# Optimization experiments

Hardware: AMD Instinct MI355X
Metric: run time of the kernel (lower is better)

## Reference

```python
import jax, jax.numpy as jnp
import numpy as np

HEAD = 16
EMB = 1024
D_K = EMB // HEAD


def setup_inputs() -> dict:
    key = jax.random.key(0)
    ks = jax.random.split(key, 11)
    B, S, E = 2, 2048, EMB
    scale = 1.0 / np.sqrt(E)
    inp = {
        "query": jax.random.normal(ks[0], (B, S, E), jnp.float32),
        "key": jax.random.normal(ks[1], (B, S, E), jnp.float32),
        "value": jax.random.normal(ks[2], (B, S, E), jnp.float32),
        "Wq": jax.random.normal(ks[3], (E, E), jnp.float32) * scale,
        "bq": jnp.zeros((E,), jnp.float32),
        "Wk": jax.random.normal(ks[4], (E, E), jnp.float32) * scale,
        "bk": jnp.zeros((E,), jnp.float32),
        "Wv": jax.random.normal(ks[5], (E, E), jnp.float32) * scale,
        "bv": jnp.zeros((E,), jnp.float32),
        "Wo": jax.random.normal(ks[6], (E, E), jnp.float32) * scale,
        "bo": jnp.zeros((E,), jnp.float32),
    }
    return inp


def reference(query, key, value, Wq, bq, Wk, bk, Wv, bv, Wo, bo):
    B, S, E = query.shape
    # 3 input projections, split into heads: [B, H, S, d_k]
    def proj(x, W, b):
        return (x @ W.T + b).reshape(B, S, HEAD, D_K).transpose(0, 2, 1, 3)

    q = proj(query, Wq, bq)
    k = proj(key, Wk, bk)
    v = proj(value, Wv, bv)

    # scaled dot-product attention (full matrix, as in original)
    scores = jnp.einsum("bhqd,bhkd->bhqk", q, k) / jnp.sqrt(jnp.float32(D_K))
    attn = jax.nn.softmax(scores, axis=-1)  # dropout in eval mode = identity
    x = jnp.einsum("bhqk,bhkd->bhqd", attn, v)

    # merge heads and output projection
    x = x.transpose(0, 2, 1, 3).reshape(B, S, E)
    return x @ Wo.T + bo
```

## Files before the change

kernel.cpp:

```cpp
#include <hip/hip_runtime.h>
#include <hip/hip_bf16.h>
#include <math.h>


constexpr int Sn = 2048;
constexpr int En = 1024;
constexpr int Hn = 16;
constexpr int Dk = 64;
constexpr int Kn = 1024;
constexpr size_t WSZ = 1048576;
constexpr size_t TSZ = 4194304;
constexpr int PST = 72;

typedef __bf16 bf16x8 __attribute__((ext_vector_type(8)));
typedef float  f32x4  __attribute__((ext_vector_type(4)));

union U16 { uint4 u; bf16x8 v; __hip_bfloat16 h[8]; };
union U8  { uint2 u; __hip_bfloat162 h2[2]; __hip_bfloat16 h[4]; };

__device__ inline U16 cvt8f(const float* __restrict__ p) {
    float4 a = *(const float4*)p;
    float4 b = *(const float4*)(p + 4);
    U16 r;
    r.h[0] = __float2bfloat16(a.x); r.h[1] = __float2bfloat16(a.y);
    r.h[2] = __float2bfloat16(a.z); r.h[3] = __float2bfloat16(a.w);
    r.h[4] = __float2bfloat16(b.x); r.h[5] = __float2bfloat16(b.y);
    r.h[6] = __float2bfloat16(b.z); r.h[7] = __float2bfloat16(b.w);
    return r;
}

__device__ inline void gload16(const __hip_bfloat16* g, __hip_bfloat16* l) {
    __builtin_amdgcn_global_load_lds(
        (const __attribute__((address_space(1))) void*)g,
        (__attribute__((address_space(3))) void*)l, 16, 0, 0);
}

template<int ROWS, int NW>
__device__ inline void stage_tile(const __hip_bfloat16* __restrict__ src, int ld,
                                  __hip_bfloat16* lds, int w, int lane) {
    int l8 = lane >> 3;
    int g = (lane & 7) ^ (l8 & 7);
    #pragma unroll
    for (int j = 0; j < ROWS / (8 * NW); ++j) {
        int c = j * NW + w;
        gload16(src + (size_t)(c * 8 + l8) * ld + g * 8, lds + c * 512);
    }
}

__global__ __launch_bounds__(256)
void cvt_w(const float* __restrict__ w0, const float* __restrict__ w1,
           const float* __restrict__ w2, const float* __restrict__ w3,
           __hip_bfloat16* __restrict__ dst)
{
    int y = blockIdx.y;
    const float* src = (y == 0) ? w0 : (y == 1) ? w1 : (y == 2) ? w2 : w3;
    size_t i = ((size_t)blockIdx.x * 256 + threadIdx.x) * 8;
    U16 r = cvt8f(src + i);
    *(uint4*)&dst[(size_t)y * WSZ + i] = r.u;
}

__global__ __launch_bounds__(256)
void cvt_x(const float* __restrict__ src, __hip_bfloat16* __restrict__ dst)
{
    size_t i = ((size_t)blockIdx.x * 256 + threadIdx.x) * 8;
    U16 r = cvt8f(src + i);
    *(uint4*)&dst[i] = r.u;
}

template<int MODE>
__global__ __launch_bounds__(256)
void gemm64(const __hip_bfloat16* __restrict__ A, const __hip_bfloat16* __restrict__ W,
            const float* __restrict__ bias, void* __restrict__ outp)
{
    __shared__ __align__(16) __hip_bfloat16 As[64 * 64];
    __shared__ __align__(16) __hip_bfloat16 Bs[128 * 64];

    const int tid = threadIdx.x, w = tid >> 6, lane = tid & 63;
    const int l15 = lane & 15, lg = lane >> 4, l7 = lane & 7;
    const int blockM = blockIdx.x * 64, blockN = blockIdx.y * 128;
    const int wm = (w & 1) * 32, wn = (w >> 1) * 64;
    const int coff0 = (lg ^ l7) * 8;
    const int coff1 = ((4 + lg) ^ l7) * 8;

    f32x4 acc[2][4];
    #pragma unroll
    for (int i = 0; i < 2; ++i)
        #pragma unroll
        for (int j = 0; j < 4; ++j) acc[i][j] = {0.f, 0.f, 0.f, 0.f};

    for (int k0 = 0; k0 < Kn; k0 += 64) {
        stage_tile<64, 4>(A + (size_t)blockM * Kn + k0, Kn, As, w, lane);
        stage_tile<128, 4>(W + (size_t)blockN * Kn + k0, Kn, Bs, w, lane);
        __syncthreads();

        U16 af[2][2], bf[4][2];
        #pragma unroll
        for (int mt = 0; mt < 2; ++mt) {
            int r = (wm + mt * 16 + l15) * 64;
            af[mt][0].u = *(const uint4*)&As[r + coff0];
            af[mt][1].u = *(const uint4*)&As[r + coff1];
        }
        #pragma unroll
        for (int nt = 0; nt < 4; ++nt) {
            int r = (wn + nt * 16 + l15) * 64;
            bf[nt][0].u = *(const uint4*)&Bs[r + coff0];
            bf[nt][1].u = *(const uint4*)&Bs[r + coff1];
        }
        #pragma unroll
        for (int mt = 0; mt < 2; ++mt)
            #pragma unroll
            for (int nt = 0; nt < 4; ++nt) {
                acc[mt][nt] = __builtin_amdgcn_mfma_f32_16x16x32_bf16(af[mt][0].v, bf[nt][0].v, acc[mt][nt], 0, 0, 0);
                acc[mt][nt] = __builtin_amdgcn_mfma_f32_16x16x32_bf16(af[mt][1].v, bf[nt][1].v, acc[mt][nt], 0, 0, 0);
            }
        __syncthreads();
    }

    #pragma unroll
    for (int nt = 0; nt < 4; ++nt) {
        int n = blockN + wn + nt * 16 + l15;
        float bvn = bias[n];
        int h_ = n >> 6, d_ = n & 63;
        #pragma unroll
        for (int mt = 0; mt < 2; ++mt) {
            int m0 = blockM + wm + mt * 16 + lg * 4;
            if constexpr (MODE == 0) {
                float* out = (float*)outp;
                #pragma unroll
                for (int i = 0; i < 4; ++i)
                    out[(size_t)(m0 + i) * Kn + n] = acc[mt][nt][i] + bvn;
            } else if constexpr (MODE == 1) {
                __hip_bfloat16* out = (__hip_bfloat16*)outp;
                int b_ = m0 >> 11, s_ = m0 & (Sn - 1);
                #pragma unroll
                for (int i = 0; i < 4; ++i)
                    out[(((size_t)b_ * Hn + h_) * Sn + s_ + i) * Dk + d_] =
                        __float2bfloat16(acc[mt][nt][i] + bvn);
            } else {
                __hip_bfloat16* out = (__hip_bfloat16*)outp;
                int b_ = m0 >> 11, s_ = m0 & (Sn - 1);
                U8 pk;
                #pragma unroll
                for (int i = 0; i < 4; ++i) pk.h[i] = __float2bfloat16(acc[mt][nt][i] + bvn);
                *(uint2*)&out[(((size_t)b_ * Hn + h_) * Dk + d_) * Sn + s_] = pk.u;
            }
        }
    }
}

__global__ __launch_bounds__(256)
void attn(const __hip_bfloat16* __restrict__ Q, const __hip_bfloat16* __restrict__ K,
          const __hip_bfloat16* __restrict__ Vt, __hip_bfloat16* __restrict__ X)
{
    __shared__ __align__(16) __hip_bfloat16 Ks[2][64 * 64];
    __shared__ __align__(16) __hip_bfloat16 Vts[2][64 * 64];
    __shared__ __align__(16) __hip_bfloat16 Ps[128 * PST];

    const int bh = blockIdx.y, q0 = blockIdx.x * 128;
    const int tid = threadIdx.x, w = tid >> 6, lane = tid & 63;
    const int l15 = lane & 15, lg = lane >> 4, l7 = lane & 7;
    const int coff0 = (lg ^ l7) * 8;
    const int coff1 = ((4 + lg) ^ l7) * 8;

    const __hip_bfloat16* Qb = Q  + (size_t)bh * Sn * Dk;
    const __hip_bfloat16* Kb = K  + (size_t)bh * Sn * Dk;
    const __hip_bfloat16* Vb = Vt + (size_t)bh * Dk * Sn;

    U16 aq[2][2];
    #pragma unroll
    for (int qt = 0; qt < 2; ++qt) {
        const __hip_bfloat16* qp = Qb + (size_t)(q0 + w * 32 + qt * 16 + l15) * Dk + lg * 8;
        aq[qt][0].u = *(const uint4*)qp;
        aq[qt][1].u = *(const uint4*)(qp + 32);
    }

    f32x4 o[2][4];
    float lpart[2];
    #pragma unroll
    for (int qt = 0; qt < 2; ++qt) {
        lpart[qt] = 0.f;
        #pragma unroll
        for (int dt = 0; dt < 4; ++dt) o[qt][dt] = {0.f, 0.f, 0.f, 0.f};
    }

    __hip_bfloat16* Pw = Ps + (w * 32) * PST;

    stage_tile<64, 4>(Kb, Dk, Ks[0], w, lane);
    stage_tile<64, 4>(Vb, Sn, Vts[0], w, lane);

    for (int t = 0; t < Sn / 64; ++t) {
        __syncthreads();
        const int cur = t & 1;
        if (t + 1 < Sn / 64) {
            stage_tile<64, 4>(Kb + (size_t)(t + 1) * 64 * Dk, Dk, Ks[cur ^ 1], w, lane);
            stage_tile<64, 4>(Vb + (t + 1) * 64, Sn, Vts[cur ^ 1], w, lane);
        }

        U16 kf[4][2];
        #pragma unroll
        for (int kt = 0; kt < 4; ++kt) {
            int r = (kt * 16 + l15) * 64;
            kf[kt][0].u = *(const uint4*)&Ks[cur][r + coff0];
            kf[kt][1].u = *(const uint4*)&Ks[cur][r + coff1];
        }
        #pragma unroll
        for (int kt = 0; kt < 4; ++kt)
            #pragma unroll
            for (int qt = 0; qt < 2; ++qt) {
                f32x4 s = {0.f, 0.f, 0.f, 0.f};
                s = __builtin_amdgcn_mfma_f32_16x16x32_bf16(kf[kt][0].v, aq[qt][0].v, s, 0, 0, 0);
                s = __builtin_amdgcn_mfma_f32_16x16x32_bf16(kf[kt][1].v, aq[qt][1].v, s, 0, 0, 0);
                float p0 = __expf(s[0] * 0.125f), p1 = __expf(s[1] * 0.125f);
                float p2 = __expf(s[2] * 0.125f), p3 = __expf(s[3] * 0.125f);
                lpart[qt] += (p0 + p1) + (p2 + p3);
                U8 pk;
                pk.h2[0] = __float22bfloat162_rn({p0, p1});
                pk.h2[1] = __float22bfloat162_rn({p2, p3});
                *(uint2*)&Pw[(qt * 16 + l15) * PST + kt * 16 + lg * 4] = pk.u;
            }

        U16 pf[2][2], vf[4][2];
        #pragma unroll
        for (int qt = 0; qt < 2; ++qt) {
            const __hip_bfloat16* pr = &Pw[(qt * 16 + l15) * PST + lg * 8];
            pf[qt][0].u = *(const uint4*)pr;
            pf[qt][1].u = *(const uint4*)(pr + 32);
        }
        #pragma unroll
        for (int dt = 0; dt < 4; ++dt) {
            int r = (dt * 16 + l15) * 64;
            vf[dt][0].u = *(const uint4*)&Vts[cur][r + coff0];
            vf[dt][1].u = *(const uint4*)&Vts[cur][r + coff1];
        }
        #pragma unroll
        for (int qt = 0; qt < 2; ++qt)
            #pragma unroll
            for (int dt = 0; dt < 4; ++dt) {
                o[qt][dt] = __builtin_amdgcn_mfma_f32_16x16x32_bf16(pf[qt][0].v, vf[dt][0].v, o[qt][dt], 0, 0, 0);
                o[qt][dt] = __builtin_amdgcn_mfma_f32_16x16x32_bf16(pf[qt][1].v, vf[dt][1].v, o[qt][dt], 0, 0, 0);
            }
    }

    float linv[2][4];
    #pragma unroll
    for (int qt = 0; qt < 2; ++qt) {
        float v = lpart[qt];
        v += __shfl_xor(v, 16, 64);
        v += __shfl_xor(v, 32, 64);
        #pragma unroll
        for (int i = 0; i < 4; ++i)
            linv[qt][i] = 1.f / __shfl(v, lg * 4 + i, 16);
    }

    int b_ = bh >> 4, h_ = bh & (Hn - 1);
    #pragma unroll
    for (int qt = 0; qt < 2; ++qt)
        #pragma unroll
        for (int i = 0; i < 4; ++i) {
            int sr = q0 + w * 32 + qt * 16 + lg * 4 + i;
            __hip_bfloat16* xp = X + ((size_t)(b_ * Sn + sr)) * En + h_ * Dk + l15;
            #pragma unroll
            for (int dt = 0; dt < 4; ++dt)
                xp[dt * 16] = __float2bfloat16(o[qt][dt][i] * linv[qt][i]);
        }
}

extern "C" void kernel_launch(void* const* d_in, const int* in_sizes, int n_in,
                              void* d_out, int out_size, void* d_ws, size_t ws_size,
                              hipStream_t stream)
{
    const float* query = (const float*)d_in[0];
    const float* key   = (const float*)d_in[1];
    const float* value = (const float*)d_in[2];
    const float* Wq = (const float*)d_in[3];
    const float* bq = (const float*)d_in[4];
    const float* Wk = (const float*)d_in[5];
    const float* bk = (const float*)d_in[6];
    const float* Wv = (const float*)d_in[7];
    const float* bv = (const float*)d_in[8];
    const float* Wo = (const float*)d_in[9];
    const float* bo = (const float*)d_in[10];
    float* out = (float*)d_out;

    __hip_bfloat16* xbuf = (__hip_bfloat16*)d_ws;
    __hip_bfloat16* Wbf  = xbuf + TSZ;
    __hip_bfloat16* Qw   = Wbf + 4 * WSZ;
    __hip_bfloat16* Kw   = Qw + TSZ;
    __hip_bfloat16* Vtw  = Kw + TSZ;
    __hip_bfloat16* Xw   = xbuf;

    dim3 ggrid(64, 8);

    cvt_w<<<dim3(512, 4), 256, 0, stream>>>(Wq, Wk, Wv, Wo, Wbf);
    cvt_x<<<2048, 256, 0, stream>>>(query, xbuf);
    gemm64<1><<<ggrid, 256, 0, stream>>>(xbuf, Wbf, bq, Qw);
    cvt_x<<<2048, 256, 0, stream>>>(key, xbuf);
    gemm64<1><<<ggrid, 256, 0, stream>>>(xbuf, Wbf + WSZ, bk, Kw);
    cvt_x<<<2048, 256, 0, stream>>>(value, xbuf);
    gemm64<2><<<ggrid, 256, 0, stream>>>(xbuf, Wbf + 2 * WSZ, bv, Vtw);
    attn<<<dim3(Sn / 128, 32), 256, 0, stream>>>(Qw, Kw, Vtw, Xw);
    gemm64<0><<<ggrid, 256, 0, stream>>>(Xw, Wbf + 3 * WSZ, bo, out);
}
```

Measured before the change: 245.5 us.

## Fold softmax scale into Q, use exp2, MFMA row sums, single-buffer K/V

```diff
diff --git a/kernel.cpp b/kernel.cpp
--- a/kernel.cpp
+++ b/kernel.cpp
@@ -70,7 +70,7 @@
 template<int MODE>
 __global__ __launch_bounds__(256)
 void gemm64(const __hip_bfloat16* __restrict__ A, const __hip_bfloat16* __restrict__ W,
-            const float* __restrict__ bias, void* __restrict__ outp)
+            const float* __restrict__ bias, void* __restrict__ outp, float scale)
 {
     __shared__ __align__(16) __hip_bfloat16 As[64 * 64];
     __shared__ __align__(16) __hip_bfloat16 Bs[128 * 64];
@@ -135,7 +135,7 @@
                 #pragma unroll
                 for (int i = 0; i < 4; ++i)
                     out[(((size_t)b_ * Hn + h_) * Sn + s_ + i) * Dk + d_] =
-                        __float2bfloat16(acc[mt][nt][i] + bvn);
+                        __float2bfloat16((acc[mt][nt][i] + bvn) * scale);
             } else {
                 __hip_bfloat16* out = (__hip_bfloat16*)outp;
                 int b_ = m0 >> 11, s_ = m0 & (Sn - 1);
@@ -152,8 +152,8 @@
 void attn(const __hip_bfloat16* __restrict__ Q, const __hip_bfloat16* __restrict__ K,
           const __hip_bfloat16* __restrict__ Vt, __hip_bfloat16* __restrict__ X)
 {
-    __shared__ __align__(16) __hip_bfloat16 Ks[2][64 * 64];
-    __shared__ __align__(16) __hip_bfloat16 Vts[2][64 * 64];
+    __shared__ __align__(16) __hip_bfloat16 Ks[64 * 64];
+    __shared__ __align__(16) __hip_bfloat16 Vts[64 * 64];
     __shared__ __align__(16) __hip_bfloat16 Ps[128 * PST];
 
     const int bh = blockIdx.y, q0 = blockIdx.x * 128;
@@ -166,6 +166,13 @@
     const __hip_bfloat16* Kb = K  + (size_t)bh * Sn * Dk;
     const __hip_bfloat16* Vb = Vt + (size_t)bh * Dk * Sn;
 
+    U16 onesf;
+    {
+        __hip_bfloat16 v = (l15 == 0) ? __float2bfloat16(1.0f) : __float2bfloat16(0.0f);
+        #pragma unroll
+        for (int j = 0; j < 8; ++j) onesf.h[j] = v;
+    }
+
     U16 aq[2][2];
     #pragma unroll
     for (int qt = 0; qt < 2; ++qt) {
@@ -175,33 +182,27 @@
     }
 
     f32x4 o[2][4];
-    float lpart[2];
+    f32x4 o4[2];
     #pragma unroll
     for (int qt = 0; qt < 2; ++qt) {
-        lpart[qt] = 0.f;
+        o4[qt] = {0.f, 0.f, 0.f, 0.f};
         #pragma unroll
         for (int dt = 0; dt < 4; ++dt) o[qt][dt] = {0.f, 0.f, 0.f, 0.f};
     }
 
     __hip_bfloat16* Pw = Ps + (w * 32) * PST;
 
-    stage_tile<64, 4>(Kb, Dk, Ks[0], w, lane);
-    stage_tile<64, 4>(Vb, Sn, Vts[0], w, lane);
-
     for (int t = 0; t < Sn / 64; ++t) {
+        stage_tile<64, 4>(Kb + (size_t)t * 64 * Dk, Dk, Ks, w, lane);
+        stage_tile<64, 4>(Vb + t * 64, Sn, Vts, w, lane);
         __syncthreads();
-        const int cur = t & 1;
-        if (t + 1 < Sn / 64) {
-            stage_tile<64, 4>(Kb + (size_t)(t + 1) * 64 * Dk, Dk, Ks[cur ^ 1], w, lane);
-            stage_tile<64, 4>(Vb + (t + 1) * 64, Sn, Vts[cur ^ 1], w, lane);
-        }
 
         U16 kf[4][2];
         #pragma unroll
         for (int kt = 0; kt < 4; ++kt) {
             int r = (kt * 16 + l15) * 64;
-            kf[kt][0].u = *(const uint4*)&Ks[cur][r + coff0];
-            kf[kt][1].u = *(const uint4*)&Ks[cur][r + coff1];
+            kf[kt][0].u = *(const uint4*)&Ks[r + coff0];
+            kf[kt][1].u = *(const uint4*)&Ks[r + coff1];
         }
         #pragma unroll
         for (int kt = 0; kt < 4; ++kt)
@@ -210,12 +211,9 @@
                 f32x4 s = {0.f, 0.f, 0.f, 0.f};
                 s = __builtin_amdgcn_mfma_f32_16x16x32_bf16(kf[kt][0].v, aq[qt][0].v, s, 0, 0, 0);
                 s = __builtin_amdgcn_mfma_f32_16x16x32_bf16(kf[kt][1].v, aq[qt][1].v, s, 0, 0, 0);
-                float p0 = __expf(s[0] * 0.125f), p1 = __expf(s[1] * 0.125f);
-                float p2 = __expf(s[2] * 0.125f), p3 = __expf(s[3] * 0.125f);
-                lpart[qt] += (p0 + p1) + (p2 + p3);
                 U8 pk;
-                pk.h2[0] = __float22bfloat162_rn({p0, p1});
-                pk.h2[1] = __float22bfloat162_rn({p2, p3});
+                pk.h2[0] = __float22bfloat162_rn({exp2f(s[0]), exp2f(s[1])});
+                pk.h2[1] = __float22bfloat162_rn({exp2f(s[2]), exp2f(s[3])});
                 *(uint2*)&Pw[(qt * 16 + l15) * PST + kt * 16 + lg * 4] = pk.u;
             }
 
@@ -229,28 +227,28 @@
         #pragma unroll
         for (int dt = 0; dt < 4; ++dt) {
             int r = (dt * 16 + l15) * 64;
-            vf[dt][0].u = *(const uint4*)&Vts[cur][r + coff0];
-            vf[dt][1].u = *(const uint4*)&Vts[cur][r + coff1];
-        }
-        #pragma unroll
-        for (int qt = 0; qt < 2; ++qt)
+            vf[dt][0].u = *(const uint4*)&Vts[r + coff0];
+            vf[dt][1].u = *(const uint4*)&Vts[r + coff1];
+        }
+        #pragma unroll
+        for (int qt = 0; qt < 2; ++qt) {
             #pragma unroll
             for (int dt = 0; dt < 4; ++dt) {
                 o[qt][dt] = __builtin_amdgcn_mfma_f32_16x16x32_bf16(pf[qt][0].v, vf[dt][0].v, o[qt][dt], 0, 0, 0);
                 o[qt][dt] = __builtin_amdgcn_mfma_f32_16x16x32_bf16(pf[qt][1].v, vf[dt][1].v, o[qt][dt], 0, 0, 0);
             }
+            o4[qt] = __builtin_amdgcn_mfma_f32_16x16x32_bf16(pf[qt][0].v, onesf.v, o4[qt], 0, 0, 0);
+            o4[qt] = __builtin_amdgcn_mfma_f32_16x16x32_bf16(pf[qt][1].v, onesf.v, o4[qt], 0, 0, 0);
+        }
+        __syncthreads();
     }
 
     float linv[2][4];
     #pragma unroll
-    for (int qt = 0; qt < 2; ++qt) {
-        float v = lpart[qt];
-        v += __shfl_xor(v, 16, 64);
-        v += __shfl_xor(v, 32, 64);
+    for (int qt = 0; qt < 2; ++qt)
         #pragma unroll
         for (int i = 0; i < 4; ++i)
-            linv[qt][i] = 1.f / __shfl(v, lg * 4 + i, 16);
-    }
+            linv[qt][i] = 1.f / __shfl(o4[qt][i], lane & 48, 64);
 
     int b_ = bh >> 4, h_ = bh & (Hn - 1);
     #pragma unroll
@@ -289,15 +287,16 @@
     __hip_bfloat16* Vtw  = Kw + TSZ;
     __hip_bfloat16* Xw   = xbuf;
 
+    const float QSCALE = 0.125f * 1.44269504f;
     dim3 ggrid(64, 8);
 
     cvt_w<<<dim3(512, 4), 256, 0, stream>>>(Wq, Wk, Wv, Wo, Wbf);
     cvt_x<<<2048, 256, 0, stream>>>(query, xbuf);
-    gemm64<1><<<ggrid, 256, 0, stream>>>(xbuf, Wbf, bq, Qw);
+    gemm64<1><<<ggrid, 256, 0, stream>>>(xbuf, Wbf, bq, Qw, QSCALE);
     cvt_x<<<2048, 256, 0, stream>>>(key, xbuf);
-    gemm64<1><<<ggrid, 256, 0, stream>>>(xbuf, Wbf + WSZ, bk, Kw);
+    gemm64<1><<<ggrid, 256, 0, stream>>>(xbuf, Wbf + WSZ, bk, Kw, 1.0f);
     cvt_x<<<2048, 256, 0, stream>>>(value, xbuf);
-    gemm64<2><<<ggrid, 256, 0, stream>>>(xbuf, Wbf + 2 * WSZ, bv, Vtw);
+    gemm64<2><<<ggrid, 256, 0, stream>>>(xbuf, Wbf + 2 * WSZ, bv, Vtw, 1.0f);
     attn<<<dim3(Sn / 128, 32), 256, 0, stream>>>(Qw, Kw, Vtw, Xw);
-    gemm64<0><<<ggrid, 256, 0, stream>>>(Xw, Wbf + 3 * WSZ, bo, out);
-}
+    gemm64<0><<<ggrid, 256, 0, stream>>>(Xw, Wbf + 3 * WSZ, bo, out, 1.0f);
+}
```

Result: slower. 252.7 us (+2.9%).
